# Kernel tuning notes

Hardware: AMD Instinct MI355X
Metric: run time of the kernel (lower is better)

The kernel has to match this reference:

```python
import jax, jax.numpy as jnp
import numpy as np

DIM = 1024
N_HEADS = 16
D_HEAD = DIM // N_HEADS


def setup_inputs() -> dict:
    key = jax.random.key(0)
    ks = jax.random.split(key, 7)
    s = DIM ** -0.5
    return {
        "x": jax.random.normal(ks[0], (4, 2048, DIM), dtype=jnp.float32),
        "Wq": jax.random.normal(ks[1], (DIM, DIM), dtype=jnp.float32) * s,
        "bq": jax.random.normal(ks[2], (DIM,), dtype=jnp.float32) * 0.02,
        "Wk": jax.random.normal(ks[3], (DIM, DIM), dtype=jnp.float32) * s,
        "bk": jax.random.normal(ks[4], (DIM,), dtype=jnp.float32) * 0.02,
        "Wv": jax.random.normal(ks[5], (DIM, DIM), dtype=jnp.float32) * s,
        "bv": jax.random.normal(ks[6], (DIM,), dtype=jnp.float32) * 0.02,
    }


def reference(x, Wq, bq, Wk, bk, Wv, bv):
    B, N, D = x.shape
    H, Dh = N_HEADS, D_HEAD

    def split_heads(t):
        # b n (h d) -> b h n d
        return t.reshape(B, N, H, Dh).transpose(0, 2, 1, 3)

    q = split_heads(x @ Wq + bq)
    k = split_heads(x @ Wk + bk)
    v = split_heads(x @ Wv + bv)

    scale = Dh ** -0.5
    logit = jnp.einsum("bhnd,bhmd->bhnm", q, k) * scale  # [B,H,N,N]
    attn = jax.nn.softmax(logit, axis=-1)
    out = jnp.einsum("bhnm,bhmd->bhnd", attn, v)
    # b h n d -> b n (h d)
    return out.transpose(0, 2, 1, 3).reshape(B, N, D)
```

## Files before the change

kernel.cpp:

```cpp
#include <hip/hip_runtime.h>
#include <hip/hip_bf16.h>
#include <stdint.h>

#define BB 4
#define SEQ 2048
#define DIM 1024
#define NH 16
#define DH 64
#define MM (BB*SEQ)

typedef unsigned short u16;
typedef __attribute__((ext_vector_type(8))) __bf16 bf16x8;
typedef __attribute__((ext_vector_type(4))) float floatx4;
typedef __attribute__((ext_vector_type(4))) unsigned short u16x4;

#define QSCALE 0.18033688011112042f

__device__ __forceinline__ u16 f2bf(float f) {
    union { float f; unsigned u; } v; v.f = f;
    unsigned u = v.u;
    u += 0x7FFF + ((u >> 16) & 1);
    return (u16)(u >> 16);
}

__device__ __forceinline__ bf16x8 ldb8(const u16* p) {
    return *(const bf16x8*)(const void*)p;
}

__device__ __forceinline__ void async_copy16(const u16* g, u16* l) {
    __builtin_amdgcn_global_load_lds(
        (const __attribute__((address_space(1))) unsigned int*)g,
        (__attribute__((address_space(3))) unsigned int*)l, 16, 0, 0);
}

__global__ __launch_bounds__(256)
void conv_x(const float* __restrict__ x, u16* __restrict__ xb) {
    const size_t i = ((size_t)blockIdx.x * 256 + threadIdx.x) * 4;
    float4 f = *(const float4*)(x + i);
    u16x4 o = { f2bf(f.x), f2bf(f.y), f2bf(f.z), f2bf(f.w) };
    *(u16x4*)(xb + i) = o;
}

__global__ __launch_bounds__(256)
void conv_wt(const float* __restrict__ Wq, const float* __restrict__ Wk,
             const float* __restrict__ Wv, u16* __restrict__ Wt) {
    const int t = blockIdx.z;
    const float* W = (t == 0) ? Wq : (t == 1) ? Wk : Wv;
    u16* D = Wt + (size_t)t * DIM * DIM;
    __shared__ u16 T[64][65];
    const int k0 = blockIdx.x * 64, n0 = blockIdx.y * 64;
    const int tid = threadIdx.x;
    #pragma unroll
    for (int p = 0; p < 4; p++) {
        const int r = p * 16 + (tid >> 4), c = (tid & 15) * 4;
        float4 f = *(const float4*)(W + (size_t)(k0 + r) * DIM + n0 + c);
        T[c + 0][r] = f2bf(f.x); T[c + 1][r] = f2bf(f.y);
        T[c + 2][r] = f2bf(f.z); T[c + 3][r] = f2bf(f.w);
    }
    __syncthreads();
    #pragma unroll
    for (int p = 0; p < 4; p++) {
        const int rn = p * 16 + (tid >> 4), ck = (tid & 15) * 4;
        u16x4 v = { T[rn][ck], T[rn][ck + 1], T[rn][ck + 2], T[rn][ck + 3] };
        *(u16x4*)(D + (size_t)(n0 + rn) * DIM + k0 + ck) = v;
    }
}

__global__ __launch_bounds__(256)
void qkv_gemm2(const u16* __restrict__ xb, const u16* __restrict__ Wt,
               const float* __restrict__ bq, const float* __restrict__ bk,
               const float* __restrict__ bv, u16* __restrict__ ws) {
    __shared__ u16 As[128 * 32];
    __shared__ u16 Bs[128 * 32];

    const int m0 = blockIdx.x * 128;
    const int t  = blockIdx.y >> 3;
    const int c0 = (blockIdx.y & 7) * 128;
    const u16* Wtb = Wt + (size_t)t * DIM * DIM;
    const float* bias = (t == 0) ? bq : (t == 1) ? bk : bv;
    const float osc = (t == 0) ? QSCALE : 1.0f;
    u16* dst = ws + (size_t)t * ((size_t)MM * DIM);

    const int tid  = threadIdx.x;
    const int lane = tid & 63;
    const int w    = tid >> 6;
    const int wr = w >> 1, wc = w & 1;
    const int g = lane >> 4, ln = lane & 15;

    floatx4 acc[4][4];
    #pragma unroll
    for (int i = 0; i < 4; i++)
        #pragma unroll
        for (int j = 0; j < 4; j++) acc[i][j] = (floatx4){0.f,0.f,0.f,0.f};

    const int srow = w * 16 + (lane >> 2);
    const int skof = (lane & 3) * 8;

    for (int kk = 0; kk < DIM; kk += 32) {
        const u16* ga0 = xb  + (size_t)(m0 + srow)      * DIM + kk + skof;
        const u16* ga1 = xb  + (size_t)(m0 + 64 + srow) * DIM + kk + skof;
        const u16* gb0 = Wtb + (size_t)(c0 + srow)      * DIM + kk + skof;
        const u16* gb1 = Wtb + (size_t)(c0 + 64 + srow) * DIM + kk + skof;
        async_copy16(ga0, &As[w * 512]);
        async_copy16(ga1, &As[2048 + w * 512]);
        async_copy16(gb0, &Bs[w * 512]);
        async_copy16(gb1, &Bs[2048 + w * 512]);
        __syncthreads();

        bf16x8 a[4], b[4];
        #pragma unroll
        for (int fr = 0; fr < 4; fr++)
            a[fr] = ldb8(&As[(wr*64 + fr*16 + ln) * 32 + g*8]);
        #pragma unroll
        for (int fc = 0; fc < 4; fc++)
            b[fc] = ldb8(&Bs[(wc*64 + fc*16 + ln) * 32 + g*8]);

        if (t < 2) {
            #pragma unroll
            for (int fr = 0; fr < 4; fr++)
                #pragma unroll
                for (int fc = 0; fc < 4; fc++)
                    acc[fr][fc] = __builtin_amdgcn_mfma_f32_16x16x32_bf16(
                        b[fc], a[fr], acc[fr][fc], 0, 0, 0);
        } else {
            #pragma unroll
            for (int fr = 0; fr < 4; fr++)
                #pragma unroll
                for (int fc = 0; fc < 4; fc++)
                    acc[fr][fc] = __builtin_amdgcn_mfma_f32_16x16x32_bf16(
                        a[fr], b[fc], acc[fr][fc], 0, 0, 0);
        }
        __syncthreads();
    }

    if (t < 2) {
        #pragma unroll
        for (int fc = 0; fc < 4; fc++) {
            const int cc = c0 + wc*64 + fc*16 + g*4;
            const float4 b4 = *(const float4*)&bias[cc];
            const int h = cc >> 6, d = cc & 63;
            #pragma unroll
            for (int fr = 0; fr < 4; fr++) {
                const int tok = m0 + wr*64 + fr*16 + ln;
                const int bidx = tok >> 11, nn = tok & 2047;
                u16x4 v = { f2bf((acc[fr][fc][0] + b4.x) * osc),
                            f2bf((acc[fr][fc][1] + b4.y) * osc),
                            f2bf((acc[fr][fc][2] + b4.z) * osc),
                            f2bf((acc[fr][fc][3] + b4.w) * osc) };
                *(u16x4*)&dst[((size_t)(bidx*NH + h)*SEQ + nn)*DH + d] = v;
            }
        }
    } else {
        #pragma unroll
        for (int fc = 0; fc < 4; fc++) {
            const int cc = c0 + wc*64 + fc*16 + ln;
            const float bias_v = bias[cc];
            const int h = cc >> 6, d = cc & 63;
            #pragma unroll
            for (int fr = 0; fr < 4; fr++) {
                const int mrow = m0 + wr*64 + fr*16 + g*4;
                const int bidx = mrow >> 11, nn = mrow & 2047;
                u16x4 v = { f2bf(acc[fr][fc][0] + bias_v), f2bf(acc[fr][fc][1] + bias_v),
                            f2bf(acc[fr][fc][2] + bias_v), f2bf(acc[fr][fc][3] + bias_v) };
                *(u16x4*)&dst[((size_t)(bidx*NH + h)*DH + d)*SEQ + nn] = v;
            }
        }
    }
}

#define LDA 40
__global__ __launch_bounds__(256)
void qkv_gemm(const float* __restrict__ x,
              const float* __restrict__ Wq, const float* __restrict__ bq,
              const float* __restrict__ Wk, const float* __restrict__ bk,
              const float* __restrict__ Wv, const float* __restrict__ bv,
              u16* __restrict__ ws) {
    __shared__ u16 As[128 * LDA];
    __shared__ u16 Bs[128 * LDA];
    const int m0 = blockIdx.x * 128;
    const int t  = blockIdx.y >> 3;
    const int c0 = (blockIdx.y & 7) * 128;
    const float* W    = (t == 0) ? Wq : (t == 1) ? Wk : Wv;
    const float* bias = (t == 0) ? bq : (t == 1) ? bk : bv;
    const float osc = (t == 0) ? QSCALE : 1.0f;
    u16* dst = ws + (size_t)t * ((size_t)MM * DIM);
    const int tid  = threadIdx.x;
    const int lane = tid & 63;
    const int wave = tid >> 6;
    const int wr = wave >> 1, wc = wave & 1;
    const int g = lane >> 4, ln = lane & 15;
    floatx4 acc[4][4];
    #pragma unroll
    for (int i = 0; i < 4; i++)
        #pragma unroll
        for (int j = 0; j < 4; j++) acc[i][j] = (floatx4){0.f,0.f,0.f,0.f};
    const int ar  = tid >> 1;
    const int ak  = (tid & 1) * 16;
    const int bkr = tid & 31;
    const int bc  = (tid >> 5) * 16;
    for (int kk = 0; kk < DIM; kk += 32) {
        {
            const float4* s4 = (const float4*)(x + (size_t)(m0 + ar) * DIM + kk + ak);
            float4 f0 = s4[0], f1 = s4[1], f2 = s4[2], f3 = s4[3];
            unsigned pk[8];
            pk[0] = f2bf(f0.x) | ((unsigned)f2bf(f0.y) << 16);
            pk[1] = f2bf(f0.z) | ((unsigned)f2bf(f0.w) << 16);
            pk[2] = f2bf(f1.x) | ((unsigned)f2bf(f1.y) << 16);
            pk[3] = f2bf(f1.z) | ((unsigned)f2bf(f1.w) << 16);
            pk[4] = f2bf(f2.x) | ((unsigned)f2bf(f2.y) << 16);
            pk[5] = f2bf(f2.z) | ((unsigned)f2bf(f2.w) << 16);
            pk[6] = f2bf(f3.x) | ((unsigned)f2bf(f3.y) << 16);
            pk[7] = f2bf(f3.z) | ((unsigned)f2bf(f3.w) << 16);
            uint4* d = (uint4*)&As[ar * LDA + ak];
            d[0] = make_uint4(pk[0], pk[1], pk[2], pk[3]);
            d[1] = make_uint4(pk[4], pk[5], pk[6], pk[7]);
        }
        {
            const float4* s4 = (const float4*)(W + (size_t)(kk + bkr) * DIM + c0 + bc);
            float4 f0 = s4[0], f1 = s4[1], f2 = s4[2], f3 = s4[3];
            float fv[16] = {f0.x,f0.y,f0.z,f0.w, f1.x,f1.y,f1.z,f1.w,
                            f2.x,f2.y,f2.z,f2.w, f3.x,f3.y,f3.z,f3.w};
            #pragma unroll
            for (int j = 0; j < 16; j++)
                Bs[(bc + j) * LDA + bkr] = f2bf(fv[j]);
        }
        __syncthreads();
        bf16x8 a[4], b[4];
        #pragma unroll
        for (int fr = 0; fr < 4; fr++)
            a[fr] = ldb8(&As[(wr*64 + fr*16 + ln) * LDA + g*8]);
        #pragma unroll
        for (int fc = 0; fc < 4; fc++)
            b[fc] = ldb8(&Bs[(wc*64 + fc*16 + ln) * LDA + g*8]);
        #pragma unroll
        for (int fr = 0; fr < 4; fr++)
            #pragma unroll
            for (int fc = 0; fc < 4; fc++)
                acc[fr][fc] = __builtin_amdgcn_mfma_f32_16x16x32_bf16(
                    a[fr], b[fc], acc[fr][fc], 0, 0, 0);
        __syncthreads();
    }
    #pragma unroll
    for (int fc = 0; fc < 4; fc++) {
        const int cc = c0 + wc*64 + fc*16 + ln;
        const float bias_v = bias[cc];
        const int h = cc >> 6, d = cc & 63;
        #pragma unroll
        for (int fr = 0; fr < 4; fr++) {
            #pragma unroll
            for (int rr = 0; rr < 4; rr++) {
                const int mrow = m0 + wr*64 + fr*16 + g*4 + rr;
                const int bidx = mrow >> 11, nn = mrow & 2047;
                const float val = (acc[fr][fc][rr] + bias_v) * osc;
                size_t idx;
                if (t < 2) idx = ((size_t)(bidx*NH + h)*SEQ + nn)*DH + d;
                else       idx = ((size_t)(bidx*NH + h)*DH + d)*SEQ + nn;
                dst[idx] = f2bf(val);
            }
        }
    }
}

#define LDP 72

__global__ __launch_bounds__(256, 2)
void attn5(const u16* __restrict__ ws, float* __restrict__ out) {
    const int qt = blockIdx.x;
    const int h  = blockIdx.y;
    const int b  = blockIdx.z;
    const int bh = b*NH + h;

    const u16* Qw = ws;
    const u16* Kw = ws + (size_t)MM * DIM;
    const u16* Vt = ws + 2 * (size_t)MM * DIM;

    __shared__ u16 Kbuf[2][4096];
    __shared__ u16 Vbuf[2][4096];
    __shared__ u16 P[4][64 * LDP];

    const int tid  = threadIdx.x;
    const int lane = tid & 63;
    const int w    = tid >> 6;
    const int g = lane >> 4, ln = lane & 15;
    const int q0 = qt*256 + w*64;

    const int srow = w*8 + (lane >> 3);
    const int sseg = (lane & 7) ^ ((lane >> 3) & 7);
    const u16* kg = Kw + ((size_t)bh*SEQ + srow)*DH + sseg*8;
    const u16* vg = Vt + ((size_t)bh*DH + srow)*SEQ + sseg*8;

    const int fs0 = ((0*4 + g) ^ (ln & 7)) * 8;
    const int fs1 = ((1*4 + g) ^ (ln & 7)) * 8;

    bf16x8 aq[4][2];
    #pragma unroll
    for (int rb = 0; rb < 4; rb++) {
        const u16* qp = Qw + ((size_t)bh*SEQ + q0 + rb*16 + ln)*DH + g*8;
        aq[rb][0] = ldb8(qp);
        aq[rb][1] = ldb8(qp + 32);
    }

    floatx4 acc[4][4];
    #pragma unroll
    for (int rb = 0; rb < 4; rb++)
        #pragma unroll
        for (int i = 0; i < 4; i++) acc[rb][i] = (floatx4){0.f,0.f,0.f,0.f};
    float lrun[4] = {0.f, 0.f, 0.f, 0.f};

    u16* Pw = &P[w][0];

    async_copy16(kg,                  &Kbuf[0][w*512]);
    async_copy16(kg + (size_t)32*DH,  &Kbuf[0][2048 + w*512]);
    async_copy16(vg,                  &Vbuf[0][w*512]);
    async_copy16(vg + (size_t)32*SEQ, &Vbuf[0][2048 + w*512]);
    __syncthreads();

    for (int kt = 0; kt < 32; kt++) {
        const int cur = kt & 1;
        if (kt < 31) {
            const int nxt = cur ^ 1;
            const size_t ko = (size_t)(kt + 1) * 64 * DH;
            const size_t vo = (size_t)(kt + 1) * 64;
            async_copy16(kg + ko,                  &Kbuf[nxt][w*512]);
            async_copy16(kg + ko + (size_t)32*DH,  &Kbuf[nxt][2048 + w*512]);
            async_copy16(vg + vo,                  &Vbuf[nxt][w*512]);
            async_copy16(vg + vo + (size_t)32*SEQ, &Vbuf[nxt][2048 + w*512]);
        }

        const u16* Kc = &Kbuf[cur][0];
        const u16* Vc = &Vbuf[cur][0];

        bf16x8 bkf[4][2];
        #pragma unroll
        for (int fn = 0; fn < 4; fn++) {
            bkf[fn][0] = ldb8(&Kc[(fn*16 + ln)*64 + fs0]);
            bkf[fn][1] = ldb8(&Kc[(fn*16 + ln)*64 + fs1]);
        }

        #pragma unroll
        for (int rb = 0; rb < 4; rb++) {
            #pragma unroll
            for (int fn = 0; fn < 4; fn++) {
                floatx4 z = (floatx4){0.f,0.f,0.f,0.f};
                z = __builtin_amdgcn_mfma_f32_16x16x32_bf16(bkf[fn][0], aq[rb][0], z, 0, 0, 0);
                z = __builtin_amdgcn_mfma_f32_16x16x32_bf16(bkf[fn][1], aq[rb][1], z, 0, 0, 0);
                float p0 = __builtin_amdgcn_exp2f(z[0]);
                float p1 = __builtin_amdgcn_exp2f(z[1]);
                float p2 = __builtin_amdgcn_exp2f(z[2]);
                float p3 = __builtin_amdgcn_exp2f(z[3]);
                lrun[rb] += (p0 + p1) + (p2 + p3);
                __hip_bfloat162 lo = __float22bfloat162_rn(make_float2(p0, p1));
                __hip_bfloat162 hi = __float22bfloat162_rn(make_float2(p2, p3));
                union { __hip_bfloat162 v2[2]; u16x4 v4; } u;
                u.v2[0] = lo; u.v2[1] = hi;
                *(u16x4*)&Pw[(rb*16 + ln)*LDP + fn*16 + g*4] = u.v4;
            }
        }

        bf16x8 av[4][2];
        #pragma unroll
        for (int fd = 0; fd < 4; fd++) {
            av[fd][0] = ldb8(&Vc[(fd*16 + ln)*64 + fs0]);
            av[fd][1] = ldb8(&Vc[(fd*16 + ln)*64 + fs1]);
        }
        bf16x8 bp[4][2];
        #pragma unroll
        for (int rb = 0; rb < 4; rb++) {
            bp[rb][0] = ldb8(&Pw[(rb*16 + ln)*LDP + g*8]);
            bp[rb][1] = ldb8(&Pw[(rb*16 + ln)*LDP + 32 + g*8]);
        }

        #pragma unroll
        for (int fd = 0; fd < 4; fd++)
            #pragma unroll
            for (int rb = 0; rb < 4; rb++) {
                acc[rb][fd] = __builtin_amdgcn_mfma_f32_16x16x32_bf16(av[fd][0], bp[rb][0], acc[rb][fd], 0, 0, 0);
                acc[rb][fd] = __builtin_amdgcn_mfma_f32_16x16x32_bf16(av[fd][1], bp[rb][1], acc[rb][fd], 0, 0, 0);
            }

        __syncthreads();
    }

    #pragma unroll
    for (int rb = 0; rb < 4; rb++) {
        float v = lrun[rb];
        v += __shfl_xor(v, 16, 64);
        v += __shfl_xor(v, 32, 64);
        lrun[rb] = v;
    }
    #pragma unroll
    for (int rb = 0; rb < 4; rb++) {
        const float inv = 1.0f / lrun[rb];
        const int n = q0 + rb*16 + ln;
        #pragma unroll
        for (int fd = 0; fd < 4; fd++) {
            floatx4 v = acc[rb][fd];
            float4 o = { v[0]*inv, v[1]*inv, v[2]*inv, v[3]*inv };
            *(float4*)&out[((size_t)b*SEQ + n)*DIM + h*DH + fd*16 + g*4] = o;
        }
    }
}

extern "C" void kernel_launch(void* const* d_in, const int* in_sizes, int n_in,
                              void* d_out, int out_size, void* d_ws, size_t ws_size,
                              hipStream_t stream) {
    const float* x  = (const float*)d_in[0];
    const float* Wq = (const float*)d_in[1];
    const float* bq = (const float*)d_in[2];
    const float* Wk = (const float*)d_in[3];
    const float* bk = (const float*)d_in[4];
    const float* Wv = (const float*)d_in[5];
    const float* bv = (const float*)d_in[6];
    u16* ws = (u16*)d_ws;
    float* out = (float*)d_out;

    const size_t need = (size_t)4 * MM * DIM * 2 + (size_t)3 * DIM * DIM * 2;
    if (ws_size >= need) {
        u16* xb = ws + (size_t)3 * MM * DIM;
        u16* Wt = ws + (size_t)4 * MM * DIM;
        conv_x<<<dim3(MM*DIM/1024), 256, 0, stream>>>(x, xb);
        conv_wt<<<dim3(DIM/64, DIM/64, 3), 256, 0, stream>>>(Wq, Wk, Wv, Wt);
        qkv_gemm2<<<dim3(MM/128, 24), 256, 0, stream>>>(xb, Wt, bq, bk, bv, ws);
    } else {
        qkv_gemm<<<dim3(MM/128, 24), 256, 0, stream>>>(x, Wq, bq, Wk, bk, Wv, bv, ws);
    }
    attn5<<<dim3(SEQ/256, NH, BB), 256, 0, stream>>>(ws, out);
}
```

Before: 259.4 us.

## Double-buffer QKV GEMM LDS loads with swizzle and merge conversion kernels

```diff
diff --git a/kernel.cpp b/kernel.cpp
--- a/kernel.cpp
+++ b/kernel.cpp
@@ -34,22 +34,25 @@
 }
 
 __global__ __launch_bounds__(256)
-void conv_x(const float* __restrict__ x, u16* __restrict__ xb) {
-    const size_t i = ((size_t)blockIdx.x * 256 + threadIdx.x) * 4;
-    float4 f = *(const float4*)(x + i);
-    u16x4 o = { f2bf(f.x), f2bf(f.y), f2bf(f.z), f2bf(f.w) };
-    *(u16x4*)(xb + i) = o;
-}
-
-__global__ __launch_bounds__(256)
-void conv_wt(const float* __restrict__ Wq, const float* __restrict__ Wk,
-             const float* __restrict__ Wv, u16* __restrict__ Wt) {
-    const int t = blockIdx.z;
+void prep(const float* __restrict__ x, u16* __restrict__ xb,
+          const float* __restrict__ Wq, const float* __restrict__ Wk,
+          const float* __restrict__ Wv, u16* __restrict__ Wt) {
+    const int bx = blockIdx.x;
+    const int tid = threadIdx.x;
+    if (bx < 8192) {
+        const size_t i = ((size_t)bx * 256 + tid) * 4;
+        float4 f = *(const float4*)(x + i);
+        u16x4 o = { f2bf(f.x), f2bf(f.y), f2bf(f.z), f2bf(f.w) };
+        *(u16x4*)(xb + i) = o;
+        return;
+    }
+    const int idx = bx - 8192;
+    const int t = idx >> 8;
+    const int r2 = idx & 255;
+    const int k0 = (r2 >> 4) * 64, n0 = (r2 & 15) * 64;
     const float* W = (t == 0) ? Wq : (t == 1) ? Wk : Wv;
     u16* D = Wt + (size_t)t * DIM * DIM;
     __shared__ u16 T[64][65];
-    const int k0 = blockIdx.x * 64, n0 = blockIdx.y * 64;
-    const int tid = threadIdx.x;
     #pragma unroll
     for (int p = 0; p < 4; p++) {
         const int r = p * 16 + (tid >> 4), c = (tid & 15) * 4;
@@ -66,12 +69,12 @@
     }
 }
 
-__global__ __launch_bounds__(256)
-void qkv_gemm2(const u16* __restrict__ xb, const u16* __restrict__ Wt,
+__global__ __launch_bounds__(256, 3)
+void qkv_gemm3(const u16* __restrict__ xb, const u16* __restrict__ Wt,
                const float* __restrict__ bq, const float* __restrict__ bk,
                const float* __restrict__ bv, u16* __restrict__ ws) {
-    __shared__ u16 As[128 * 32];
-    __shared__ u16 Bs[128 * 32];
+    __shared__ u16 As[2][4096];
+    __shared__ u16 Bs[2][4096];
 
     const int m0 = blockIdx.x * 128;
     const int t  = blockIdx.y >> 3;
@@ -93,27 +96,37 @@
         #pragma unroll
         for (int j = 0; j < 4; j++) acc[i][j] = (floatx4){0.f,0.f,0.f,0.f};
 
-    const int srow = w * 16 + (lane >> 2);
-    const int skof = (lane & 3) * 8;
-
-    for (int kk = 0; kk < DIM; kk += 32) {
-        const u16* ga0 = xb  + (size_t)(m0 + srow)      * DIM + kk + skof;
-        const u16* ga1 = xb  + (size_t)(m0 + 64 + srow) * DIM + kk + skof;
-        const u16* gb0 = Wtb + (size_t)(c0 + srow)      * DIM + kk + skof;
-        const u16* gb1 = Wtb + (size_t)(c0 + 64 + srow) * DIM + kk + skof;
-        async_copy16(ga0, &As[w * 512]);
-        async_copy16(ga1, &As[2048 + w * 512]);
-        async_copy16(gb0, &Bs[w * 512]);
-        async_copy16(gb1, &Bs[2048 + w * 512]);
-        __syncthreads();
+    const int srow = w*16 + (lane >> 2);
+    const int gseg = (lane & 3) ^ ((lane >> 3) & 3);
+    const u16* gA = xb  + (size_t)(m0 + srow) * DIM + gseg*8;
+    const u16* gB = Wtb + (size_t)(c0 + srow) * DIM + gseg*8;
+
+    async_copy16(gA,                   &As[0][w*512]);
+    async_copy16(gA + (size_t)64*DIM,  &As[0][2048 + w*512]);
+    async_copy16(gB,                   &Bs[0][w*512]);
+    async_copy16(gB + (size_t)64*DIM,  &Bs[0][2048 + w*512]);
+    __syncthreads();
+
+    const int xu = (ln >> 1) & 3;
+
+    for (int it = 0; it < 32; it++) {
+        const int cur = it & 1;
+        if (it < 31) {
+            const int nxt = cur ^ 1;
+            const int kk = (it + 1) * 32;
+            async_copy16(gA + kk,                  &As[nxt][w*512]);
+            async_copy16(gA + kk + (size_t)64*DIM, &As[nxt][2048 + w*512]);
+            async_copy16(gB + kk,                  &Bs[nxt][w*512]);
+            async_copy16(gB + kk + (size_t)64*DIM, &Bs[nxt][2048 + w*512]);
+        }
 
         bf16x8 a[4], b[4];
         #pragma unroll
         for (int fr = 0; fr < 4; fr++)
-            a[fr] = ldb8(&As[(wr*64 + fr*16 + ln) * 32 + g*8]);
+            a[fr] = ldb8(&As[cur][(wr*64 + fr*16 + ln)*32 + (g ^ xu)*8]);
         #pragma unroll
         for (int fc = 0; fc < 4; fc++)
-            b[fc] = ldb8(&Bs[(wc*64 + fc*16 + ln) * 32 + g*8]);
+            b[fc] = ldb8(&Bs[cur][(wc*64 + fc*16 + ln)*32 + (g ^ xu)*8]);
 
         if (t < 2) {
             #pragma unroll
@@ -418,9 +431,8 @@
     if (ws_size >= need) {
         u16* xb = ws + (size_t)3 * MM * DIM;
         u16* Wt = ws + (size_t)4 * MM * DIM;
-        conv_x<<<dim3(MM*DIM/1024), 256, 0, stream>>>(x, xb);
-        conv_wt<<<dim3(DIM/64, DIM/64, 3), 256, 0, stream>>>(Wq, Wk, Wv, Wt);
-        qkv_gemm2<<<dim3(MM/128, 24), 256, 0, stream>>>(xb, Wt, bq, bk, bv, ws);
+        prep<<<dim3(8192 + 768), 256, 0, stream>>>(x, xb, Wq, Wk, Wv, Wt);
+        qkv_gemm3<<<dim3(MM/128, 24), 256, 0, stream>>>(xb, Wt, bq, bk, bv, ws);
     } else {
         qkv_gemm<<<dim3(MM/128, 24), 256, 0, stream>>>(x, Wq, bq, Wk, bk, Wv, bv, ws);
     }
```

Result: faster. 253.2 us (-2.4%).
